# Kernel tuning notes

Hardware: AMD Instinct MI355X
Metric: run time of the kernel (lower is better)

Reference implementation:

```python
import jax, jax.numpy as jnp
import numpy as np

N_RAYS = 32768
N_SAMPLES = 1048576
HID = 64
STEP = 0.0005


def _mlp(x, W1, b1, W2, b2, W3, b3):
    h = jax.nn.relu(x @ W1 + b1)
    h = jax.nn.relu(h @ W2 + b2)
    return h @ W3 + b3


def setup_inputs() -> dict:
    key = jax.random.key(0)
    ks = jax.random.split(key, 12)
    rays_o = jax.random.normal(ks[0], (N_RAYS, 3), jnp.float32)
    rays_d = jax.random.normal(ks[1], (N_RAYS, 3), jnp.float32)
    rays_d = rays_d / jnp.linalg.norm(rays_d, axis=-1, keepdims=True)
    t_starts = jax.random.uniform(ks[2], (N_SAMPLES,), jnp.float32, 0.0, 1.5)
    t_ends = t_starts + STEP
    ray_indices = jnp.sort(jax.random.randint(ks[3], (N_SAMPLES,), 0, N_RAYS, jnp.int32))
    def lin(k, fin, fout):
        return jax.random.normal(k, (fin, fout), jnp.float32) / np.sqrt(fin)
    return {
        'rays_o': rays_o, 'rays_d': rays_d,
        't_starts': t_starts, 't_ends': t_ends,
        'ray_indices': ray_indices,
        'W_d1': lin(ks[4], 3, HID), 'b_d1': jnp.zeros((HID,), jnp.float32),
        'W_d2': lin(ks[5], HID, HID), 'b_d2': jnp.zeros((HID,), jnp.float32),
        'W_d3': lin(ks[6], HID, 1), 'b_d3': jnp.zeros((1,), jnp.float32),
        'W_r1': lin(ks[7], 3, HID), 'b_r1': jnp.zeros((HID,), jnp.float32),
        'W_r2': lin(ks[8], HID, HID), 'b_r2': jnp.zeros((HID,), jnp.float32),
        'W_r3': lin(ks[9], HID, 3), 'b_r3': jnp.zeros((3,), jnp.float32),
    }


def reference(rays_o, rays_d, t_starts, t_ends, ray_indices,
              W_d1, b_d1, W_d2, b_d2, W_d3, b_d3,
              W_r1, b_r1, W_r2, b_r2, W_r3, b_r3):
    n_rays = rays_o.shape[0]
    mid = (t_starts + t_ends) * 0.5                      # [S]
    # gather ray origins/dirs per sample, compute positions
    positions = rays_o[ray_indices] + rays_d[ray_indices] * mid[:, None]  # [S,3]
    # density query (NGP decoder stand-in), softplus activation like trunc_exp family
    sigmas = jax.nn.softplus(_mlp(positions, W_d1, b_d1, W_d2, b_d2, W_d3, b_d3))[:, 0]  # [S]
    # render_weight_from_density: segment-wise exclusive cumsum of sigma*dt
    sigma_dt = sigmas * (t_ends - t_starts)              # [S]
    excl_global = jnp.cumsum(sigma_dt) - sigma_dt        # global exclusive cumsum
    per_ray = jax.ops.segment_sum(sigma_dt, ray_indices, num_segments=n_rays)  # [R]
    ray_excl = jnp.cumsum(per_ray) - per_ray             # exclusive cumsum over rays
    within_excl = excl_global - ray_excl[ray_indices]    # exclusive within each ray
    trans = jnp.exp(-within_excl)                        # transmittance
    alphas = 1.0 - jnp.exp(-sigma_dt)
    weights = trans * alphas
    # accumulate_along_rays (scatter-sum over ray_indices)
    opacities = jax.ops.segment_sum(weights, ray_indices, num_segments=n_rays)[:, None]  # [R,1]
    distances = jax.ops.segment_sum(weights * mid, ray_indices, num_segments=n_rays)[:, None]
    # rgb query
    rgbs = jax.nn.sigmoid(_mlp(positions, W_r1, b_r1, W_r2, b_r2, W_r3, b_r3))  # [S,3]
    w_sg = jax.lax.stop_gradient(weights)
    colors = jax.ops.segment_sum(w_sg[:, None] * rgbs, ray_indices, num_segments=n_rays)  # [R,3]
    # eval-mode background composition (nerf.training == False branch)
    rest = jax.lax.stop_gradient(1.0 - opacities)
    distances = distances + 5.0 * rest
    colors = colors + 0.5 * rest
    return colors, distances, opacities
```

## Files before the change

### kernel.cpp

```cpp
#include <hip/hip_runtime.h>
#include <hip/hip_bf16.h>
#include <math.h>

#define N_RAYS   32768
#define N_SAMP   1048576
#define HID      64
#define ITERS    4
#define BLK_A    1024

typedef short bf8 __attribute__((ext_vector_type(8)));
typedef float f4  __attribute__((ext_vector_type(4)));

union BF8U { bf8 v; unsigned u[4]; };

static __device__ __forceinline__ unsigned bfbits(float x) {
    union { __bf16 h; unsigned short s; } c; c.h = (__bf16)x; return (unsigned)c.s;
}
static __device__ __forceinline__ unsigned pk2(float a, float b) {
    return bfbits(a) | (bfbits(b) << 16);
}
static __device__ __forceinline__ unsigned pk2r(float a, float b) {
    return pk2(fmaxf(a, 0.f), fmaxf(b, 0.f));
}
static __device__ __forceinline__ f4 mfma16(bf8 a, bf8 b, f4 c) {
    return __builtin_amdgcn_mfma_f32_16x16x32_bf16(a, b, c, 0, 0, 0);
}

__global__ __launch_bounds__(256, 2) void pass_a(
    const float* __restrict__ rays_o, const float* __restrict__ rays_d,
    const float* __restrict__ t_starts, const float* __restrict__ t_ends,
    const int*   __restrict__ ray_idx,
    const float* __restrict__ Wd1, const float* __restrict__ bd1,
    const float* __restrict__ Wd2, const float* __restrict__ bd2,
    const float* __restrict__ Wd3, const float* __restrict__ bd3,
    const float* __restrict__ Wr1, const float* __restrict__ br1,
    const float* __restrict__ Wr2, const float* __restrict__ br2,
    const float* __restrict__ Wr3, const float* __restrict__ br3,
    float4* __restrict__ ws4, int* __restrict__ start)
{
    const int lane = threadIdx.x & 63;
    const int wv   = (blockIdx.x * blockDim.x + threadIdx.x) >> 6;
    const int q    = lane >> 4;
    const int n    = lane & 15;
    const int qn   = n >> 2, rn = n & 3;

    bf8 a1d[4], a1r[4];
    #pragma unroll
    for (int t = 0; t < 4; ++t) {
        const int row = 8*qn + 4*(t&1) + rn + 32*(t>>1);
        BF8U fd, fr;
        fd.u[0] = pk2(Wd1[row],       Wd1[HID+row]);
        fd.u[1] = pk2(Wd1[2*HID+row], bd1[row]);
        fd.u[2] = 0u; fd.u[3] = 0u;
        fr.u[0] = pk2(Wr1[row],       Wr1[HID+row]);
        fr.u[1] = pk2(Wr1[2*HID+row], br1[row]);
        fr.u[2] = 0u; fr.u[3] = 0u;
        a1d[t] = fd.v; a1r[t] = fr.v;
    }

    bf8 a2d[4][2], a2r[4][2];
    #pragma unroll
    for (int t = 0; t < 4; ++t) {
        const int row = 8*qn + 4*(t&1) + rn + 32*(t>>1);
        #pragma unroll
        for (int s = 0; s < 2; ++s) {
            BF8U fd, fr;
            #pragma unroll
            for (int dw = 0; dw < 4; ++dw) {
                const int k = 8*q + 2*dw + 32*s;
                fd.u[dw] = pk2(Wd2[k*HID+row], Wd2[(k+1)*HID+row]);
                fr.u[dw] = pk2(Wr2[k*HID+row], Wr2[(k+1)*HID+row]);
            }
            a2d[t][s] = fd.v; a2r[t][s] = fr.v;
        }
    }

    bf8 a3[4];
    #pragma unroll
    for (int s = 0; s < 4; ++s) {
        BF8U f;
        #pragma unroll
        for (int dw = 0; dw < 4; ++dw) {
            const int kg = 32*s + 8*q + 2*dw;
            float va = 0.f, vb = 0.f;
            if (n == 0 && s < 2)                 { va = Wd3[kg]; vb = Wd3[kg+1]; }
            else if (n >= 1 && n <= 3 && s >= 2) {
                va = Wr3[(kg-64)*3 + (n-1)];
                vb = Wr3[(kg-63)*3 + (n-1)];
            }
            f.u[dw] = pk2(va, vb);
        }
        a3[s] = f.v;
    }

    f4 bias2d[4], bias2r[4];
    #pragma unroll
    for (int t = 0; t < 4; ++t) {
        #pragma unroll
        for (int rr = 0; rr < 4; ++rr) {
            const int row = 8*q + 4*(t&1) + rr + 32*(t>>1);
            bias2d[t][rr] = bd2[row];
            bias2r[t][rr] = br2[row];
        }
    }
    f4 bias3;
    #pragma unroll
    for (int rr = 0; rr < 4; ++rr)
        bias3[rr] = (q == 0) ? (rr == 0 ? bd3[0] : br3[rr-1]) : 0.f;

    const int base0 = wv * (ITERS * 64);

    #pragma unroll 1
    for (int it = 0; it < ITERS; ++it) {
        const int base = base0 + it * 64;
        const int smp  = base + lane;

        const float ts = t_starts[smp], te = t_ends[smp];
        const int   ri = ray_idx[smp];
        const float mid = 0.5f*(ts+te), dt = te - ts;
        const float px = rays_o[3*ri+0] + rays_d[3*ri+0]*mid;
        const float py = rays_o[3*ri+1] + rays_d[3*ri+1]*mid;
        const float pz = rays_o[3*ri+2] + rays_d[3*ri+2]*mid;
        const unsigned p01 = pk2(px, py);
        const unsigned p23 = pk2(pz, 1.0f);

        int rp = __shfl_up(ri, 1, 64);
        if (lane == 0) rp = (smp == 0) ? -1 : ray_idx[smp-1];
        for (int rr = rp + 1; rr <= ri; ++rr) start[rr] = smp;
        if (smp == N_SAMP - 1)
            for (int rr = ri + 1; rr <= N_RAYS; ++rr) start[rr] = N_SAMP;

        #pragma unroll
        for (int u = 0; u < 4; ++u) {
            BF8U xb;
            xb.u[0] = (q == u) ? p01 : 0u;
            xb.u[1] = (q == u) ? p23 : 0u;
            xb.u[2] = 0u; xb.u[3] = 0u;

            const f4 zero = {0.f, 0.f, 0.f, 0.f};
            f4 d1d[4], d1r[4];
            #pragma unroll
            for (int t = 0; t < 4; ++t) {
                d1d[t] = mfma16(a1d[t], xb.v, zero);
                d1r[t] = mfma16(a1r[t], xb.v, zero);
            }

            bf8 b2d[2], b2r[2];
            #pragma unroll
            for (int s = 0; s < 2; ++s) {
                BF8U pd, pr;
                pd.u[0] = pk2r(d1d[2*s][0],   d1d[2*s][1]);
                pd.u[1] = pk2r(d1d[2*s][2],   d1d[2*s][3]);
                pd.u[2] = pk2r(d1d[2*s+1][0], d1d[2*s+1][1]);
                pd.u[3] = pk2r(d1d[2*s+1][2], d1d[2*s+1][3]);
                pr.u[0] = pk2r(d1r[2*s][0],   d1r[2*s][1]);
                pr.u[1] = pk2r(d1r[2*s][2],   d1r[2*s][3]);
                pr.u[2] = pk2r(d1r[2*s+1][0], d1r[2*s+1][1]);
                pr.u[3] = pk2r(d1r[2*s+1][2], d1r[2*s+1][3]);
                b2d[s] = pd.v; b2r[s] = pr.v;
            }

            f4 d2d[4], d2r[4];
            #pragma unroll
            for (int t = 0; t < 4; ++t) {
                f4 ad = bias2d[t];
                ad = mfma16(a2d[t][0], b2d[0], ad);
                ad = mfma16(a2d[t][1], b2d[1], ad);
                d2d[t] = ad;
                f4 ar = bias2r[t];
                ar = mfma16(a2r[t][0], b2r[0], ar);
                ar = mfma16(a2r[t][1], b2r[1], ar);
                d2r[t] = ar;
            }

            bf8 b3[4];
            #pragma unroll
            for (int s = 0; s < 2; ++s) {
                BF8U pd, pr;
                pd.u[0] = pk2r(d2d[2*s][0],   d2d[2*s][1]);
                pd.u[1] = pk2r(d2d[2*s][2],   d2d[2*s][3]);
                pd.u[2] = pk2r(d2d[2*s+1][0], d2d[2*s+1][1]);
                pd.u[3] = pk2r(d2d[2*s+1][2], d2d[2*s+1][3]);
                pr.u[0] = pk2r(d2r[2*s][0],   d2r[2*s][1]);
                pr.u[1] = pk2r(d2r[2*s][2],   d2r[2*s][3]);
                pr.u[2] = pk2r(d2r[2*s+1][0], d2r[2*s+1][1]);
                pr.u[3] = pk2r(d2r[2*s+1][2], d2r[2*s+1][3]);
                b3[s] = pd.v; b3[s+2] = pr.v;
            }

            f4 c3 = bias3;
            #pragma unroll
            for (int s = 0; s < 4; ++s) c3 = mfma16(a3[s], b3[s], c3);

            const float dtu = __shfl(dt, 16*u + n, 64);
            if (q == 0) {
                const float sg = c3[0];
                const float sp = fmaxf(sg, 0.f) + __logf(1.f + __expf(-fabsf(sg)));
                const float sd = sp * dtu;
                const float r0 = __builtin_amdgcn_rcpf(1.f + __expf(-c3[1]));
                const float g0 = __builtin_amdgcn_rcpf(1.f + __expf(-c3[2]));
                const float b0 = __builtin_amdgcn_rcpf(1.f + __expf(-c3[3]));
                ws4[base + 16*u + n] = make_float4(r0, g0, b0, sd);
            }
        }
    }
}

__global__ __launch_bounds__(256) void pass_b(
    const float* __restrict__ t_starts, const float* __restrict__ t_ends,
    const float4* __restrict__ ws4, const int* __restrict__ start,
    float* __restrict__ out)
{
    const int lane = threadIdx.x & 63;
    const int r    = (blockIdx.x * blockDim.x + threadIdx.x) >> 6;
    if (r >= N_RAYS) return;

    const int s0 = start[r], s1 = start[r+1];

    float cum = 0.f, opac = 0.f, dist = 0.f, c0 = 0.f, c1 = 0.f, c2 = 0.f;

    for (int base = s0; base < s1; base += 64) {
        int s = base + lane;
        bool ok = s < s1;
        float4 v = ok ? ws4[s] : make_float4(0.f, 0.f, 0.f, 0.f);
        float mid = ok ? 0.5f*(t_starts[s] + t_ends[s]) : 0.f;
        float sd = v.w;

        float x = sd;
        #pragma unroll
        for (int off = 1; off < 64; off <<= 1) {
            float y = __shfl_up(x, off, 64);
            if (lane >= off) x += y;
        }
        float excl  = x - sd;
        float trans = __expf(-(cum + excl));
        float w     = trans * (-expm1f(-sd));
        opac += w; dist += w*mid;
        c0 += w*v.x; c1 += w*v.y; c2 += w*v.z;
        cum += __shfl(x, 63, 64);
    }

    #pragma unroll
    for (int off = 32; off > 0; off >>= 1) {
        opac += __shfl_xor(opac, off, 64);
        dist += __shfl_xor(dist, off, 64);
        c0   += __shfl_xor(c0,   off, 64);
        c1   += __shfl_xor(c1,   off, 64);
        c2   += __shfl_xor(c2,   off, 64);
    }

    if (lane == 0) {
        float rest = 1.f - opac;
        out[r*3 + 0] = c0 + 0.5f * rest;
        out[r*3 + 1] = c1 + 0.5f * rest;
        out[r*3 + 2] = c2 + 0.5f * rest;
        out[3*N_RAYS + r] = dist + 5.f * rest;
        out[4*N_RAYS + r] = opac;
    }
}

extern "C" void kernel_launch(void* const* d_in, const int* in_sizes, int n_in,
                              void* d_out, int out_size, void* d_ws, size_t ws_size,
                              hipStream_t stream) {
    const float* rays_o   = (const float*)d_in[0];
    const float* rays_d   = (const float*)d_in[1];
    const float* t_starts = (const float*)d_in[2];
    const float* t_ends   = (const float*)d_in[3];
    const int*   ray_idx  = (const int*)  d_in[4];
    const float* Wd1 = (const float*)d_in[5];  const float* bd1 = (const float*)d_in[6];
    const float* Wd2 = (const float*)d_in[7];  const float* bd2 = (const float*)d_in[8];
    const float* Wd3 = (const float*)d_in[9];  const float* bd3 = (const float*)d_in[10];
    const float* Wr1 = (const float*)d_in[11]; const float* br1 = (const float*)d_in[12];
    const float* Wr2 = (const float*)d_in[13]; const float* br2 = (const float*)d_in[14];
    const float* Wr3 = (const float*)d_in[15]; const float* br3 = (const float*)d_in[16];

    float4* ws4   = (float4*)d_ws;
    int*    start = (int*)((char*)d_ws + (size_t)N_SAMP * 16);
    float*  out   = (float*)d_out;

    hipLaunchKernelGGL(pass_a, dim3(BLK_A), dim3(256), 0, stream,
                       rays_o, rays_d, t_starts, t_ends, ray_idx,
                       Wd1, bd1, Wd2, bd2, Wd3, bd3,
                       Wr1, br1, Wr2, br2, Wr3, br3, ws4, start);

    hipLaunchKernelGGL(pass_b, dim3((N_RAYS*64)/256), dim3(256), 0, stream,
                       t_starts, t_ends, ws4, start, out);
}
```

Before: 163.9 us.

## Spread MLP epilogue across all lanes and process two rays per wave in pass B

In pass A, the third-layer weights are replicated so every lane quadrant computes the output head. Each lane then keeps its own sample's result, so the softplus/sigmoid epilogue and the store run on all 64 lanes once per iteration instead of on 16 lanes four times. A packed bf16 conversion builtin is used when available, and the occupancy hint rises to 4 blocks per CU. Pass B assigns two rays per wave using 32-lane scans, rewrites the weights as a difference of transmittances, and computes opacity by telescoping, which removes one reduction. The risks are register pressure at the higher occupancy and small changes to floating-point rounding.

```diff
diff --git a/kernel.cpp b/kernel.cpp
--- a/kernel.cpp
+++ b/kernel.cpp
@@ -17,7 +17,11 @@
     union { __bf16 h; unsigned short s; } c; c.h = (__bf16)x; return (unsigned)c.s;
 }
 static __device__ __forceinline__ unsigned pk2(float a, float b) {
+#if __has_builtin(__builtin_amdgcn_cvt_pk_bf16_f32)
+    return __builtin_bit_cast(unsigned, __builtin_amdgcn_cvt_pk_bf16_f32(a, b));
+#else
     return bfbits(a) | (bfbits(b) << 16);
+#endif
 }
 static __device__ __forceinline__ unsigned pk2r(float a, float b) {
     return pk2(fmaxf(a, 0.f), fmaxf(b, 0.f));
@@ -26,7 +30,7 @@
     return __builtin_amdgcn_mfma_f32_16x16x32_bf16(a, b, c, 0, 0, 0);
 }
 
-__global__ __launch_bounds__(256, 2) void pass_a(
+__global__ __launch_bounds__(256, 4) void pass_a(
     const float* __restrict__ rays_o, const float* __restrict__ rays_d,
     const float* __restrict__ t_starts, const float* __restrict__ t_ends,
     const int*   __restrict__ ray_idx,
@@ -43,6 +47,7 @@
     const int q    = lane >> 4;
     const int n    = lane & 15;
     const int qn   = n >> 2, rn = n & 3;
+    const int rt   = n & 3;
 
     bf8 a1d[4], a1r[4];
     #pragma unroll
@@ -83,10 +88,10 @@
         for (int dw = 0; dw < 4; ++dw) {
             const int kg = 32*s + 8*q + 2*dw;
             float va = 0.f, vb = 0.f;
-            if (n == 0 && s < 2)                 { va = Wd3[kg]; vb = Wd3[kg+1]; }
-            else if (n >= 1 && n <= 3 && s >= 2) {
-                va = Wr3[(kg-64)*3 + (n-1)];
-                vb = Wr3[(kg-63)*3 + (n-1)];
+            if (rt == 0 && s < 2) { va = Wd3[kg]; vb = Wd3[kg+1]; }
+            else if (rt >= 1 && s >= 2) {
+                va = Wr3[(kg-64)*3 + (rt-1)];
+                vb = Wr3[(kg-63)*3 + (rt-1)];
             }
             f.u[dw] = pk2(va, vb);
         }
@@ -106,7 +111,7 @@
     f4 bias3;
     #pragma unroll
     for (int rr = 0; rr < 4; ++rr)
-        bias3[rr] = (q == 0) ? (rr == 0 ? bd3[0] : br3[rr-1]) : 0.f;
+        bias3[rr] = (rr == 0) ? bd3[0] : br3[rr-1];
 
     const int base0 = wv * (ITERS * 64);
 
@@ -129,6 +134,8 @@
         for (int rr = rp + 1; rr <= ri; ++rr) start[rr] = smp;
         if (smp == N_SAMP - 1)
             for (int rr = ri + 1; rr <= N_RAYS; ++rr) start[rr] = N_SAMP;
+
+        f4 mine = {0.f, 0.f, 0.f, 0.f};
 
         #pragma unroll
         for (int u = 0; u < 4; ++u) {
@@ -192,17 +199,16 @@
             #pragma unroll
             for (int s = 0; s < 4; ++s) c3 = mfma16(a3[s], b3[s], c3);
 
-            const float dtu = __shfl(dt, 16*u + n, 64);
-            if (q == 0) {
-                const float sg = c3[0];
-                const float sp = fmaxf(sg, 0.f) + __logf(1.f + __expf(-fabsf(sg)));
-                const float sd = sp * dtu;
-                const float r0 = __builtin_amdgcn_rcpf(1.f + __expf(-c3[1]));
-                const float g0 = __builtin_amdgcn_rcpf(1.f + __expf(-c3[2]));
-                const float b0 = __builtin_amdgcn_rcpf(1.f + __expf(-c3[3]));
-                ws4[base + 16*u + n] = make_float4(r0, g0, b0, sd);
-            }
-        }
+            if (q == u) mine = c3;
+        }
+
+        const float sg = mine[0];
+        const float sp = fmaxf(sg, 0.f) + __logf(1.f + __expf(-fabsf(sg)));
+        const float sd = sp * dt;
+        const float r0 = __builtin_amdgcn_rcpf(1.f + __expf(-mine[1]));
+        const float g0 = __builtin_amdgcn_rcpf(1.f + __expf(-mine[2]));
+        const float b0 = __builtin_amdgcn_rcpf(1.f + __expf(-mine[3]));
+        ws4[smp] = make_float4(r0, g0, b0, sd);
     }
 }
 
@@ -212,44 +218,48 @@
     float* __restrict__ out)
 {
     const int lane = threadIdx.x & 63;
-    const int r    = (blockIdx.x * blockDim.x + threadIdx.x) >> 6;
+    const int wv   = (blockIdx.x * blockDim.x + threadIdx.x) >> 6;
+    const int half = lane >> 5;
+    const int l32  = lane & 31;
+    const int r    = 2*wv + half;
     if (r >= N_RAYS) return;
 
     const int s0 = start[r], s1 = start[r+1];
 
     float cum = 0.f, opac = 0.f, dist = 0.f, c0 = 0.f, c1 = 0.f, c2 = 0.f;
 
-    for (int base = s0; base < s1; base += 64) {
-        int s = base + lane;
+    for (int base = s0; base < s1; base += 32) {
+        int s = base + l32;
         bool ok = s < s1;
-        float4 v = ok ? ws4[s] : make_float4(0.f, 0.f, 0.f, 0.f);
+        float4 v  = ok ? ws4[s] : make_float4(0.f, 0.f, 0.f, 0.f);
         float mid = ok ? 0.5f*(t_starts[s] + t_ends[s]) : 0.f;
-        float sd = v.w;
+        float sd  = v.w;
 
         float x = sd;
         #pragma unroll
-        for (int off = 1; off < 64; off <<= 1) {
-            float y = __shfl_up(x, off, 64);
-            if (lane >= off) x += y;
-        }
-        float excl  = x - sd;
-        float trans = __expf(-(cum + excl));
-        float w     = trans * (-expm1f(-sd));
-        opac += w; dist += w*mid;
-        c0 += w*v.x; c1 += w*v.y; c2 += w*v.z;
-        cum += __shfl(x, 63, 64);
-    }
-
-    #pragma unroll
-    for (int off = 32; off > 0; off >>= 1) {
-        opac += __shfl_xor(opac, off, 64);
-        dist += __shfl_xor(dist, off, 64);
-        c0   += __shfl_xor(c0,   off, 64);
-        c1   += __shfl_xor(c1,   off, 64);
-        c2   += __shfl_xor(c2,   off, 64);
-    }
-
-    if (lane == 0) {
+        for (int off = 1; off < 32; off <<= 1) {
+            float y = __shfl_up(x, off, 32);
+            if (l32 >= off) x += y;
+        }
+        float incl = cum + x;
+        float excl = incl - sd;
+        float w = __expf(-excl) - __expf(-incl);
+        dist += w*mid; c0 += w*v.x; c1 += w*v.y; c2 += w*v.z;
+
+        float tot = __shfl(x, 31, 32);
+        opac += __expf(-cum) - __expf(-(cum + tot));
+        cum  += tot;
+    }
+
+    #pragma unroll
+    for (int off = 16; off > 0; off >>= 1) {
+        dist += __shfl_xor(dist, off, 32);
+        c0   += __shfl_xor(c0,   off, 32);
+        c1   += __shfl_xor(c1,   off, 32);
+        c2   += __shfl_xor(c2,   off, 32);
+    }
+
+    if (l32 == 0) {
         float rest = 1.f - opac;
         out[r*3 + 0] = c0 + 0.5f * rest;
         out[r*3 + 1] = c1 + 0.5f * rest;
@@ -283,6 +293,6 @@
                        Wd1, bd1, Wd2, bd2, Wd3, bd3,
                        Wr1, br1, Wr2, br2, Wr3, br3, ws4, start);
 
-    hipLaunchKernelGGL(pass_b, dim3((N_RAYS*64)/256), dim3(256), 0, stream,
+    hipLaunchKernelGGL(pass_b, dim3((N_RAYS/2 * 64) / 256), dim3(256), 0, stream,
                        t_starts, t_ends, ws4, start, out);
 }
```

New measurement: 408.5 us. +149.2%, slower.
